# Performance work log

Hardware: AMD Instinct MI355X
Metric: run time of the kernel (lower is better)

## Reference

```python
import jax, jax.numpy as jnp
import numpy as np

B, L, T, E, H = 64, 256, 32, 384, 6
DI, DS, DC, DR = 768, 16, 4, 24  # d_inner, d_state, d_conv, dt_rank
HID, V, ND = 1536, 97, 12       # ffn hidden, num_classes, mamba depth
EPS = 1e-5


def setup_inputs() -> dict:
    key = jax.random.key(0)
    ks = jax.random.split(key, 16)
    n = lambda i, shape, s=0.02: jax.random.normal(ks[i], shape, jnp.float32) * s
    # sinusoidal position table (deterministic buffer)
    pos = np.arange(T)[:, None]
    i = np.arange(E)[None, :]
    ang = pos / np.power(10000.0, 2 * (i // 2) / E)
    pos_emb = jnp.asarray(np.where(i % 2 == 0, np.sin(ang), np.cos(ang)), jnp.float32)
    # standard S4D-real init for A_log
    Alog = jnp.log(jnp.broadcast_to(jnp.arange(1, DS + 1, dtype=jnp.float32), (ND, DI, DS)))
    return {
        'enc': jax.random.normal(ks[0], (B, L, E), jnp.float32),
        'query_embed': n(1, (1, T, E)),
        'pos_emb': pos_emb,
        'm_norm_w': jnp.ones((ND, E)),
        'm_in_w': n(2, (ND, 2 * DI, E)),
        'm_conv_w': n(3, (ND, DI, DC), 0.3),
        'm_conv_b': jnp.zeros((ND, DI)),
        'm_xproj_w': n(4, (ND, DR + 2 * DS, DI)),
        'm_dt_w': n(5, (ND, DI, DR), 0.1),
        'm_dt_b': n(6, (ND, DI), 0.5),
        'm_Alog': Alog,
        'm_D': jnp.ones((ND, DI)),
        'm_out_w': n(7, (ND, E, DI)),
        'rms_w': jnp.ones((E,)),
        'wq': n(8, (E, E)), 'bq': jnp.zeros((E,)),
        'wk': n(9, (E, E)), 'bk': jnp.zeros((E,)),
        'wv': n(10, (E, E)), 'bv': jnp.zeros((E,)),
        'wo': n(11, (E, E)), 'bo': jnp.zeros((E,)),
        'ln1_w': jnp.ones((E,)), 'ln1_b': jnp.zeros((E,)),
        'ffn_w1': n(12, (HID, E)), 'ffn_b1': jnp.zeros((HID,)),
        'ffn_w2': n(13, (E, HID)), 'ffn_b2': jnp.zeros((E,)),
        'ln2_w': jnp.ones((E,)), 'ln2_b': jnp.zeros((E,)),
        'out_w': n(14, (V, E)), 'out_b': jnp.zeros((V,)),
    }


def _rmsnorm(x, w):
    x = x.astype(jnp.float32)
    return x * jax.lax.rsqrt(jnp.mean(x * x, -1, keepdims=True) + EPS) * w


def _layernorm(x, w, b):
    x = x.astype(jnp.float32)
    mu = jnp.mean(x, -1, keepdims=True)
    var = jnp.mean((x - mu) ** 2, -1, keepdims=True)
    return (x - mu) * jax.lax.rsqrt(var + EPS) * w + b


def _mamba(x, in_w, conv_w, conv_b, xproj_w, dt_w, dt_b, Alog, Dp, ow):
    # x: (B, T, E)
    xz = jnp.einsum('bte,de->btd', x, in_w)
    xm, z = jnp.split(xz, 2, axis=-1)              # (B, T, DI) each
    t = xm.shape[1]
    xpad = jnp.pad(xm, ((0, 0), (DC - 1, 0), (0, 0)))  # causal depthwise conv
    xc = sum(conv_w[:, k] * xpad[:, k:k + t, :] for k in range(DC)) + conv_b
    xc = jax.nn.silu(xc)
    dbl = jnp.einsum('btd,rd->btr', xc, xproj_w)
    dt = jax.nn.softplus(jnp.einsum('btr,dr->btd', dbl[..., :DR], dt_w) + dt_b)
    Bm = dbl[..., DR:DR + DS]                      # (B, T, DS)
    Cm = dbl[..., DR + DS:]                        # (B, T, DS)
    A = -jnp.exp(Alog)                             # (DI, DS)
    dA = jnp.exp(dt[..., None] * A)                # (B, T, DI, DS)
    dBx = dt[..., None] * Bm[:, :, None, :] * xc[..., None]

    def step(h, inp):
        dA_t, dBx_t, C_t = inp
        h = dA_t * h + dBx_t                       # (B, DI, DS)
        return h, jnp.einsum('bds,bs->bd', h, C_t)

    h0 = jnp.zeros((xm.shape[0], DI, DS), jnp.float32)
    _, ys = jax.lax.scan(step, h0, (dA.transpose(1, 0, 2, 3), dBx.transpose(1, 0, 2, 3), Cm.transpose(1, 0, 2)))
    y = ys.transpose(1, 0, 2) + Dp * xc
    y = y * jax.nn.silu(z)
    return jnp.einsum('btd,ed->bte', y, ow)


def _block(carry, p):
    hidden, residual = carry
    norm_w, in_w, conv_w, conv_b, xproj_w, dt_w, dt_b, Alog, Dp, ow = p
    residual = hidden.astype(jnp.float32) + residual   # fused add-norm, residual_in_fp32
    hidden = _rmsnorm(residual, norm_w)
    hidden = _mamba(hidden, in_w, conv_w, conv_b, xproj_w, dt_w, dt_b, Alog, Dp, ow)
    return (hidden, residual), None


def reference(enc, query_embed, pos_emb, m_norm_w, m_in_w, m_conv_w, m_conv_b,
              m_xproj_w, m_dt_w, m_dt_b, m_Alog, m_D, m_out_w, rms_w,
              wq, bq, wk, bk, wv, bv, wo, bo, ln1_w, ln1_b,
              ffn_w1, ffn_b1, ffn_w2, ffn_b2, ln2_w, ln2_b, out_w, out_b):
    b = enc.shape[0]
    q = jnp.broadcast_to(query_embed, (b,) + query_embed.shape[1:]) + pos_emb  # (B, T, E)

    carry = (q, jnp.zeros_like(q))
    (hidden, residual), _ = jax.lax.scan(
        jax.checkpoint(_block), carry,
        (m_norm_w, m_in_w, m_conv_w, m_conv_b, m_xproj_w, m_dt_w, m_dt_b, m_Alog, m_D, m_out_w))

    # final fused RMSNorm (prenorm)
    residual = hidden + residual
    hidden = _rmsnorm(residual, rms_w)

    # cross attention: query=hidden, key=value=enc
    hd = E // H
    qh = (hidden @ wq.T + bq).reshape(b, T, H, hd)
    kh = (enc @ wk.T + bk).reshape(b, L, H, hd)
    vh = (enc @ wv.T + bv).reshape(b, L, H, hd)
    scores = jnp.einsum('bthd,bshd->bhts', qh, kh) / jnp.sqrt(jnp.float32(hd))
    attn = jax.nn.softmax(scores, axis=-1)
    ctx = jnp.einsum('bhts,bshd->bthd', attn, vh).reshape(b, T, E)
    ctx = ctx @ wo.T + bo

    residual = residual + ctx
    hidden = _layernorm(residual, ln1_w, ln1_b)

    ff = jax.nn.relu(hidden @ ffn_w1.T + ffn_b1) @ ffn_w2.T + ffn_b2
    residual = residual + ff
    hidden = _layernorm(residual, ln2_w, ln2_b)

    logits = hidden @ out_w.T + out_b              # (B, T, V)
    return logits
```

## Files before the change

### kernel.cpp

```cpp
#include <hip/hip_runtime.h>
#include <math.h>

constexpr int B_ = 64, L_ = 256, T_ = 32, E_ = 384, H_ = 6;
constexpr int DI_ = 768, DS_ = 16, DC_ = 4, DR_ = 24;
constexpr int HID_ = 1536, V_ = 97, ND_ = 12;
constexpr float EPS_ = 1e-5f;
constexpr int HD_ = 64;

typedef unsigned short ushort_t;
typedef __attribute__((ext_vector_type(8))) short  short8;
typedef __attribute__((ext_vector_type(4))) float  floatx4;
typedef __attribute__((ext_vector_type(8))) unsigned short ushort8v;

__device__ __forceinline__ float siluf(float x) { return x / (1.f + __expf(-x)); }
__device__ __forceinline__ float softplusf(float x) {
    return fmaxf(x, 0.f) + log1pf(expf(-fabsf(x)));
}
__device__ __forceinline__ ushort_t f2bf(float f) {
    unsigned int u = __float_as_uint(f);
    u += 0x7fffu + ((u >> 16) & 1u);
    return (ushort_t)(u >> 16);
}
__device__ __forceinline__ float bf2f(ushort_t u) {
    return __uint_as_float(((unsigned int)u) << 16);
}
__device__ __forceinline__ void unpack2(unsigned int w, float& lo, float& hi) {
    lo = __uint_as_float(w << 16);
    hi = __uint_as_float(w & 0xffff0000u);
}
__device__ __forceinline__ void gl_lds16(const ushort_t* g, ushort_t* l) {
    __builtin_amdgcn_global_load_lds(
        (const __attribute__((address_space(1))) unsigned int*)g,
        (__attribute__((address_space(3))) unsigned int*)l, 16, 0, 0);
}

__global__ __launch_bounds__(256) void cvt_bf16_kernel(
    const float* __restrict__ src, ushort_t* __restrict__ dst, long n4) {
    long i = (long)blockIdx.x * 256 + threadIdx.x;
    if (i >= n4) return;
    float4 v = ((const float4*)src)[i];
    __attribute__((ext_vector_type(4))) unsigned short o;
    o[0] = f2bf(v.x); o[1] = f2bf(v.y); o[2] = f2bf(v.z); o[3] = f2bf(v.w);
    *(__attribute__((ext_vector_type(4))) unsigned short*)(dst + i * 4) = o;
}

__global__ __launch_bounds__(256) void cvt_pad_kernel(
    const float* __restrict__ src, ushort_t* __restrict__ dst,
    int sr, int sc, int dr, int dc, int layers) {
    long total = (long)layers * dr * dc;
    long idx = (long)blockIdx.x * 256 + threadIdx.x;
    if (idx >= total) return;
    int l = (int)(idx / ((long)dr * dc));
    int rem = (int)(idx % ((long)dr * dc));
    int r = rem / dc, c = rem % dc;
    float v = (r < sr && c < sc) ? src[((long)l * sr + r) * sc + c] : 0.f;
    dst[idx] = f2bf(v);
}

template <int ACT, int OBF>
__global__ __launch_bounds__(256) void gemm_bf16(
    const ushort_t* __restrict__ A, int lda,
    const ushort_t* __restrict__ W,
    const float* __restrict__ bias,
    const float* __restrict__ addin,
    void* __restrict__ Cv,
    int M, int N, int K, int Nz, int ldc) {
    __shared__ ushort_t As[64 * 64];
    __shared__ ushort_t Bs[64 * 64];

    const int tid = threadIdx.x;
    const int wv = tid >> 6, ln = tid & 63;
    const int bm = blockIdx.x * 64, bn = blockIdx.y * 64;
    const int lm = ln & 15, quad = ln >> 4;
    const int wm = (wv & 1) * 32, wn = (wv >> 1) * 32;
    const int r8 = ln >> 3, c8 = ln & 7;

    floatx4 acc[2][2] = {};

    for (int k0 = 0; k0 < K; k0 += 64) {
#pragma unroll
        for (int j = 0; j < 2; ++j) {
            int row = wv * 16 + j * 8 + r8;
            int cg = c8 ^ (row & 7);
            gl_lds16(A + (size_t)(bm + row) * lda + k0 + cg * 8,
                     &As[(wv * 16 + j * 8) * 64]);
        }
#pragma unroll
        for (int j = 0; j < 2; ++j) {
            int row = wv * 16 + j * 8 + r8;
            int cg = c8 ^ (row & 7);
            gl_lds16(W + (size_t)(bn + row) * K + k0 + cg * 8,
                     &Bs[(wv * 16 + j * 8) * 64]);
        }
        __syncthreads();
#pragma unroll
        for (int ks2 = 0; ks2 < 2; ++ks2) {
            int pc = ((quad + ks2 * 4) ^ (lm & 7)) * 8;
            short8 a0 = *(const short8*)&As[(wm + lm) * 64 + pc];
            short8 a1 = *(const short8*)&As[(wm + 16 + lm) * 64 + pc];
            short8 b0 = *(const short8*)&Bs[(wn + lm) * 64 + pc];
            short8 b1 = *(const short8*)&Bs[(wn + 16 + lm) * 64 + pc];
            acc[0][0] = __builtin_amdgcn_mfma_f32_16x16x32_bf16(a0, b0, acc[0][0], 0, 0, 0);
            acc[0][1] = __builtin_amdgcn_mfma_f32_16x16x32_bf16(a0, b1, acc[0][1], 0, 0, 0);
            acc[1][0] = __builtin_amdgcn_mfma_f32_16x16x32_bf16(a1, b0, acc[1][0], 0, 0, 0);
            acc[1][1] = __builtin_amdgcn_mfma_f32_16x16x32_bf16(a1, b1, acc[1][1], 0, 0, 0);
        }
        __syncthreads();
    }

#pragma unroll
    for (int sm = 0; sm < 2; ++sm) {
#pragma unroll
        for (int sn = 0; sn < 2; ++sn) {
            const int gn = bn + wn + sn * 16 + lm;
            if (gn >= Nz) continue;
#pragma unroll
            for (int r = 0; r < 4; ++r) {
                const int gm = bm + wm + sm * 16 + quad * 4 + r;
                float v;
                if (gn < N) {
                    v = acc[sm][sn][r];
                    if (bias) v += bias[gn];
                    if (ACT == 1) v = fmaxf(v, 0.f);
                    if (ACT == 2) v = softplusf(v);
                    if (addin) v += addin[(size_t)gm * ldc + gn];
                } else {
                    v = 0.f;
                }
                if (OBF)
                    ((ushort_t*)Cv)[(size_t)gm * ldc + gn] = f2bf(v);
                else
                    ((float*)Cv)[(size_t)gm * ldc + gn] = v;
            }
        }
    }
}

__global__ __launch_bounds__(256) void gemm_in_conv(
    const ushort_t* __restrict__ A,
    const ushort_t* __restrict__ W,
    const float* __restrict__ cw,
    const float* __restrict__ cb,
    ushort_t* __restrict__ xz,
    ushort_t* __restrict__ xc) {
    __shared__ ushort_t As[64 * 64];
    __shared__ ushort_t Bs[64 * 64];
    __shared__ float Cb[64][65];
    __shared__ float Cw[64][4];
    __shared__ float Cbias[64];

    const int tid = threadIdx.x;
    const int wv = tid >> 6, ln = tid & 63;
    const int bm = blockIdx.x * 64, bn = blockIdx.y * 64;
    const int lm = ln & 15, quad = ln >> 4;
    const int wm = (wv & 1) * 32, wn = (wv >> 1) * 32;
    const int r8 = ln >> 3, c8 = ln & 7;
    const bool is_xm = (bn < DI_);

    if (is_xm && tid < 64) {
        *(float4*)&Cw[tid][0] = *(const float4*)&cw[(bn + tid) * 4];
        Cbias[tid] = cb[bn + tid];
    }

    floatx4 acc[2][2] = {};

    for (int k0 = 0; k0 < E_; k0 += 64) {
#pragma unroll
        for (int j = 0; j < 2; ++j) {
            int row = wv * 16 + j * 8 + r8;
            int cg = c8 ^ (row & 7);
            gl_lds16(A + (size_t)(bm + row) * E_ + k0 + cg * 8,
                     &As[(wv * 16 + j * 8) * 64]);
        }
#pragma unroll
        for (int j = 0; j < 2; ++j) {
            int row = wv * 16 + j * 8 + r8;
            int cg = c8 ^ (row & 7);
            gl_lds16(W + (size_t)(bn + row) * E_ + k0 + cg * 8,
                     &Bs[(wv * 16 + j * 8) * 64]);
        }
        __syncthreads();
#pragma unroll
        for (int ks2 = 0; ks2 < 2; ++ks2) {
            int pc = ((quad + ks2 * 4) ^ (lm & 7)) * 8;
            short8 a0 = *(const short8*)&As[(wm + lm) * 64 + pc];
            short8 a1 = *(const short8*)&As[(wm + 16 + lm) * 64 + pc];
            short8 b0 = *(const short8*)&Bs[(wn + lm) * 64 + pc];
            short8 b1 = *(const short8*)&Bs[(wn + 16 + lm) * 64 + pc];
            acc[0][0] = __builtin_amdgcn_mfma_f32_16x16x32_bf16(a0, b0, acc[0][0], 0, 0, 0);
            acc[0][1] = __builtin_amdgcn_mfma_f32_16x16x32_bf16(a0, b1, acc[0][1], 0, 0, 0);
            acc[1][0] = __builtin_amdgcn_mfma_f32_16x16x32_bf16(a1, b0, acc[1][0], 0, 0, 0);
            acc[1][1] = __builtin_amdgcn_mfma_f32_16x16x32_bf16(a1, b1, acc[1][1], 0, 0, 0);
        }
        __syncthreads();
    }

    if (is_xm) {
#pragma unroll
        for (int sm = 0; sm < 2; ++sm)
#pragma unroll
            for (int sn = 0; sn < 2; ++sn)
#pragma unroll
                for (int r = 0; r < 4; ++r)
                    Cb[wm + sm * 16 + quad * 4 + r][wn + sn * 16 + lm] = acc[sm][sn][r];
        __syncthreads();
        const int r = tid >> 2, c0 = (tid & 3) * 16;
        const int tl = r & 31;
        ushort_t pk[16];
#pragma unroll
        for (int j = 0; j < 16; ++j) {
            const int c = c0 + j;
            float a = Cbias[c];
#pragma unroll
            for (int k = 0; k < DC_; ++k) {
                int rr = tl + k - (DC_ - 1);
                if (rr >= 0) a += Cw[c][k] * Cb[r + k - (DC_ - 1)][c];
            }
            pk[j] = f2bf(siluf(a));
        }
        ushort_t* dst = xc + (size_t)(bm + r) * DI_ + bn + c0;
        *(ushort8v*)dst = *(ushort8v*)&pk[0];
        *(ushort8v*)(dst + 8) = *(ushort8v*)&pk[8];
    } else {
#pragma unroll
        for (int sm = 0; sm < 2; ++sm)
#pragma unroll
            for (int sn = 0; sn < 2; ++sn) {
                const int gn = bn + wn + sn * 16 + lm;
#pragma unroll
                for (int r = 0; r < 4; ++r) {
                    const int gm = bm + wm + sm * 16 + quad * 4 + r;
                    xz[(size_t)gm * 1536 + gn] = f2bf(acc[sm][sn][r]);
                }
            }
    }
}

__global__ __launch_bounds__(256) void xproj_dt_scan_kernel(
    const ushort_t* __restrict__ xc,
    const ushort_t* __restrict__ xz,
    const ushort_t* __restrict__ w_xproj,
    const float* __restrict__ dt_w,
    const float* __restrict__ dt_b,
    const float* __restrict__ Alog,
    const float* __restrict__ Dp,
    ushort_t* __restrict__ y) {
    __shared__ ushort_t Xs[32 * 768];
    __shared__ float Dbl[32][64];

    const int tid = threadIdx.x;
    const int wv = tid >> 6, ln = tid & 63;
    const int b = blockIdx.y;
    const int lm = ln & 15, quad = ln >> 4;
    const int r8 = ln >> 3, c8 = ln & 7;

#pragma unroll
    for (int i = 0; i < 12; ++i) {
        int q = wv * 96 + i * 8 + r8;
        int row = q / 12, chunk = q % 12;
        int cg = c8 ^ (row & 7);
        gl_lds16(xc + (size_t)(b * T_ + row) * DI_ + chunk * 64 + cg * 8,
                 &Xs[(wv * 96 + i * 8) * 64]);
    }
    __syncthreads();

    {
        const int mt = wv & 1, nt0 = wv >> 1;
        floatx4 a0 = {}, a1 = {};
        const int arow = mt * 16 + lm;
#pragma unroll
        for (int ks = 0; ks < 24; ++ks) {
            int og = (((ks & 1) * 4 + quad) ^ (arow & 7)) * 8;
            short8 av = *(const short8*)&Xs[(arow * 12 + (ks >> 1)) * 64 + og];
            short8 b0 = *(const short8*)(w_xproj + (size_t)(nt0 * 16 + lm) * DI_ +
                                         ks * 32 + quad * 8);
            short8 b1 = *(const short8*)(w_xproj + (size_t)((nt0 + 2) * 16 + lm) * DI_ +
                                         ks * 32 + quad * 8);
            a0 = __builtin_amdgcn_mfma_f32_16x16x32_bf16(av, b0, a0, 0, 0, 0);
            a1 = __builtin_amdgcn_mfma_f32_16x16x32_bf16(av, b1, a1, 0, 0, 0);
        }
#pragma unroll
        for (int r = 0; r < 4; ++r) {
            Dbl[mt * 16 + quad * 4 + r][nt0 * 16 + lm] = a0[r];
            Dbl[mt * 16 + quad * 4 + r][(nt0 + 2) * 16 + lm] = a1[r];
        }
    }
    __syncthreads();

    const int d = blockIdx.x * 256 + tid;
    float wdt[DR_];
#pragma unroll
    for (int r = 0; r < DR_; ++r) wdt[r] = dt_w[(size_t)d * DR_ + r];
    const float dtb_v = dt_b[d];
    float Aa[DS_];
#pragma unroll
    for (int s = 0; s < DS_; ++s) Aa[s] = -expf(Alog[(size_t)d * DS_ + s]);
    const float Dv = Dp[d];
    float h[DS_] = {};

    const int chunk64 = d >> 6, off = d & 63, elem = off & 7;
    for (int t = 0; t < T_; ++t) {
        float dtv = dtb_v;
#pragma unroll
        for (int r4 = 0; r4 < DR_ / 4; ++r4) {
            float4 dv = *(const float4*)&Dbl[t][r4 * 4];
            dtv += dv.x * wdt[r4 * 4] + dv.y * wdt[r4 * 4 + 1] +
                   dv.z * wdt[r4 * 4 + 2] + dv.w * wdt[r4 * 4 + 3];
        }
        dtv = softplusf(dtv);

        int og = ((off >> 3) ^ (t & 7)) * 8;
        float xcv = bf2f(Xs[(t * 12 + chunk64) * 64 + og + elem]);

        float acc = 0.f;
#pragma unroll
        for (int s4 = 0; s4 < DS_ / 4; ++s4) {
            float4 Bv = *(const float4*)&Dbl[t][DR_ + s4 * 4];
            float4 Cv = *(const float4*)&Dbl[t][DR_ + DS_ + s4 * 4];
#pragma unroll
            for (int j = 0; j < 4; ++j) {
                int s = s4 * 4 + j;
                float Bvj = (j == 0) ? Bv.x : (j == 1) ? Bv.y : (j == 2) ? Bv.z : Bv.w;
                float Cvj = (j == 0) ? Cv.x : (j == 1) ? Cv.y : (j == 2) ? Cv.z : Cv.w;
                h[s] = __expf(dtv * Aa[s]) * h[s] + dtv * Bvj * xcv;
                acc += h[s] * Cvj;
            }
        }
        float zv = bf2f(xz[(size_t)(b * T_ + t) * (2 * DI_) + DI_ + d]);
        y[(size_t)(b * T_ + t) * DI_ + d] = f2bf((acc + Dv * xcv) * siluf(zv));
    }
}

__global__ void init_kernel(const float* __restrict__ qe,
                            const float* __restrict__ pos,
                            float* __restrict__ houtf,
                            float* __restrict__ residual) {
    long idx = (long)blockIdx.x * 256 + threadIdx.x;
    if (idx >= (long)B_ * T_ * E_) return;
    int te = (int)(idx % ((long)T_ * E_));
    houtf[idx] = qe[te] + pos[te];
    residual[idx] = 0.f;
}

__global__ __launch_bounds__(256) void add_rmsnorm_kernel(
    const float* __restrict__ hin, float* __restrict__ residual,
    ushort_t* __restrict__ hout, const float* __restrict__ w) {
    const int row = blockIdx.x, tid = threadIdx.x;
    const long base = (long)row * E_;
    __shared__ float ws[4];

    float x0 = hin[base + tid] + residual[base + tid];
    bool has1 = (tid + 256 < E_);
    float x1 = has1 ? hin[base + tid + 256] + residual[base + tid + 256] : 0.f;
    residual[base + tid] = x0;
    if (has1) residual[base + tid + 256] = x1;

    float p = x0 * x0 + x1 * x1;
#pragma unroll
    for (int m = 1; m < 64; m <<= 1) p += __shfl_xor(p, m, 64);
    if ((tid & 63) == 0) ws[tid >> 6] = p;
    __syncthreads();
    float sc = rsqrtf((ws[0] + ws[1] + ws[2] + ws[3]) / E_ + EPS_);
    hout[base + tid] = f2bf(x0 * sc * w[tid]);
    if (has1) hout[base + tid + 256] = f2bf(x1 * sc * w[tid + 256]);
}

__global__ __launch_bounds__(256) void layernorm_kernel(
    const float* __restrict__ x, const float* __restrict__ w,
    const float* __restrict__ b, ushort_t* __restrict__ out) {
    const int row = blockIdx.x, tid = threadIdx.x;
    const long base = (long)row * E_;
    __shared__ float wa[4], wb[4];

    float x0 = x[base + tid];
    bool has1 = (tid + 256 < E_);
    float x1 = has1 ? x[base + tid + 256] : 0.f;

    float p = x0 + x1;
#pragma unroll
    for (int m = 1; m < 64; m <<= 1) p += __shfl_xor(p, m, 64);
    if ((tid & 63) == 0) wa[tid >> 6] = p;
    __syncthreads();
    float mu = (wa[0] + wa[1] + wa[2] + wa[3]) / E_;

    float d0 = x0 - mu, d1 = has1 ? x1 - mu : 0.f;
    float q = d0 * d0 + d1 * d1;
#pragma unroll
    for (int m = 1; m < 64; m <<= 1) q += __shfl_xor(q, m, 64);
    if ((tid & 63) == 0) wb[tid >> 6] = q;
    __syncthreads();
    float sc = rsqrtf((wb[0] + wb[1] + wb[2] + wb[3]) / E_ + EPS_);
    out[base + tid] = f2bf(d0 * sc * w[tid] + b[tid]);
    if (has1) out[base + tid + 256] = f2bf(d1 * sc * w[tid + 256] + b[tid + 256]);
}

__global__ __launch_bounds__(256) void attn_kernel(
    const ushort_t* __restrict__ qh,
    const ushort_t* __restrict__ kh,
    const ushort_t* __restrict__ vh,
    ushort_t* __restrict__ ctx) {
    const int h = blockIdx.x % H_;
    const int b = blockIdx.x / H_;
    const int tid = threadIdx.x;
    const int w = tid >> 6, ln = tid & 63;
    const int lm = ln & 15, quad = ln >> 4;

    __shared__ __attribute__((aligned(16))) ushort_t Vt[64 * 264];
    __shared__ __attribute__((aligned(16))) ushort_t Pb[32 * 264];
    __shared__ float rmax[4][32];
    __shared__ float rsum[4][32];

    short8 aq[2][2];
#pragma unroll
    for (int mt = 0; mt < 2; ++mt)
#pragma unroll
        for (int ks = 0; ks < 2; ++ks)
            aq[mt][ks] = *(const short8*)(qh + (size_t)(b * T_ + mt * 16 + lm) * E_ +
                                          h * HD_ + ks * 32 + quad * 8);

    short8 bk[4][2];
#pragma unroll
    for (int nt = 0; nt < 4; ++nt)
#pragma unroll
        for (int ks = 0; ks < 2; ++ks)
            bk[nt][ks] = *(const short8*)(kh + (size_t)(b * L_ + w * 64 + nt * 16 + lm) * E_ +
                                          h * HD_ + ks * 32 + quad * 8);

    {
        const int sp = tid & 127, dh = tid >> 7;
        const int s0 = sp * 2;
        const ushort_t* vr = vh + (size_t)(b * L_ + s0) * E_ + h * HD_ + dh * 32;
        uint4 va[4], vb[4];
#pragma unroll
        for (int c = 0; c < 4; ++c) {
            va[c] = *(const uint4*)(vr + c * 8);
            vb[c] = *(const uint4*)(vr + E_ + c * 8);
        }
#pragma unroll
        for (int c = 0; c < 4; ++c) {
            const unsigned int* pa = (const unsigned int*)&va[c];
            const unsigned int* pb = (const unsigned int*)&vb[c];
#pragma unroll
            for (int j = 0; j < 4; ++j) {
                int d0 = dh * 32 + c * 8 + j * 2;
                unsigned int lo = (pa[j] & 0xffffu) | (pb[j] << 16);
                unsigned int hi = (pa[j] >> 16) | (pb[j] & 0xffff0000u);
                *(unsigned int*)&Vt[d0 * 264 + s0] = lo;
                *(unsigned int*)&Vt[(d0 + 1) * 264 + s0] = hi;
            }
        }
    }

    floatx4 acc[2][4] = {};
#pragma unroll
    for (int ks = 0; ks < 2; ++ks)
#pragma unroll
        for (int mt = 0; mt < 2; ++mt)
#pragma unroll
            for (int nt = 0; nt < 4; ++nt)
                acc[mt][nt] = __builtin_amdgcn_mfma_f32_16x16x32_bf16(
                    aq[mt][ks], bk[nt][ks], acc[mt][nt], 0, 0, 0);
#pragma unroll
    for (int mt = 0; mt < 2; ++mt)
#pragma unroll
        for (int nt = 0; nt < 4; ++nt)
            acc[mt][nt] *= 0.125f;

    float mpart[2][4];
#pragma unroll
    for (int mt = 0; mt < 2; ++mt)
#pragma unroll
        for (int r = 0; r < 4; ++r) {
            float m = fmaxf(fmaxf(acc[mt][0][r], acc[mt][1][r]),
                            fmaxf(acc[mt][2][r], acc[mt][3][r]));
#pragma unroll
            for (int mk = 1; mk < 16; mk <<= 1)
                m = fmaxf(m, __shfl_xor(m, mk, 64));
            mpart[mt][r] = m;
        }
    if (lm == 0) {
#pragma unroll
        for (int mt = 0; mt < 2; ++mt)
#pragma unroll
            for (int r = 0; r < 4; ++r)
                rmax[w][mt * 16 + quad * 4 + r] = mpart[mt][r];
    }
    __syncthreads();

    float spart[2][4];
#pragma unroll
    for (int mt = 0; mt < 2; ++mt)
#pragma unroll
        for (int r = 0; r < 4; ++r) {
            const int t = mt * 16 + quad * 4 + r;
            float gm = fmaxf(fmaxf(rmax[0][t], rmax[1][t]),
                             fmaxf(rmax[2][t], rmax[3][t]));
            float s = 0.f;
#pragma unroll
            for (int nt = 0; nt < 4; ++nt) {
                float e = __expf(acc[mt][nt][r] - gm);
                s += e;
                Pb[t * 264 + w * 64 + nt * 16 + lm] = f2bf(e);
            }
#pragma unroll
            for (int mk = 1; mk < 16; mk <<= 1)
                s += __shfl_xor(s, mk, 64);
            spart[mt][r] = s;
        }
    if (lm == 0) {
#pragma unroll
        for (int mt = 0; mt < 2; ++mt)
#pragma unroll
            for (int r = 0; r < 4; ++r)
                rsum[w][mt * 16 + quad * 4 + r] = spart[mt][r];
    }
    __syncthreads();

    const int mt = w & 1, nth = w >> 1;
    floatx4 pacc[2] = {};
#pragma unroll
    for (int ks = 0; ks < 8; ++ks) {
        short8 pa = *(const short8*)&Pb[(mt * 16 + lm) * 264 + ks * 32 + quad * 8];
#pragma unroll
        for (int i = 0; i < 2; ++i) {
            short8 vb = *(const short8*)&Vt[((nth * 2 + i) * 16 + lm) * 264 + ks * 32 + quad * 8];
            pacc[i] = __builtin_amdgcn_mfma_f32_16x16x32_bf16(pa, vb, pacc[i], 0, 0, 0);
        }
    }

#pragma unroll
    for (int r = 0; r < 4; ++r) {
        const int t = mt * 16 + quad * 4 + r;
        float dn = 1.f / (rsum[0][t] + rsum[1][t] + rsum[2][t] + rsum[3][t]);
#pragma unroll
        for (int i = 0; i < 2; ++i) {
            const int d = (nth * 2 + i) * 16 + lm;
            ctx[(size_t)(b * T_ + t) * E_ + h * HD_ + d] = f2bf(pacc[i][r] * dn);
        }
    }
}

static void gemm(hipStream_t s, int act, int obf, const ushort_t* A, int lda,
                 const ushort_t* W, const float* bias, const float* addin,
                 void* C, int M, int N, int K, int Nz, int ldc) {
    dim3 g(M / 64, (Nz + 63) / 64), b(256);
    if (obf) {
        switch (act) {
            case 0: gemm_bf16<0, 1><<<g, b, 0, s>>>(A, lda, W, bias, addin, C, M, N, K, Nz, ldc); break;
            case 1: gemm_bf16<1, 1><<<g, b, 0, s>>>(A, lda, W, bias, addin, C, M, N, K, Nz, ldc); break;
            case 2: gemm_bf16<2, 1><<<g, b, 0, s>>>(A, lda, W, bias, addin, C, M, N, K, Nz, ldc); break;
        }
    } else {
        gemm_bf16<0, 0><<<g, b, 0, s>>>(A, lda, W, bias, addin, C, M, N, K, Nz, ldc);
    }
}

static void cvt(hipStream_t s, const float* src, ushort_t* dst, long n) {
    long n4 = n / 4;
    cvt_bf16_kernel<<<(int)((n4 + 255) / 256), 256, 0, s>>>(src, dst, n4);
}
static void cvt_pad(hipStream_t s, const float* src, ushort_t* dst,
                    int sr, int sc, int dr, int dc, int layers) {
    long total = (long)layers * dr * dc;
    cvt_pad_kernel<<<(int)((total + 255) / 256), 256, 0, s>>>(src, dst, sr, sc, dr, dc, layers);
}

extern "C" void kernel_launch(void* const* d_in, const int* in_sizes, int n_in,
                              void* d_out, int out_size, void* d_ws, size_t ws_size,
                              hipStream_t stream) {
    const float* enc      = (const float*)d_in[0];
    const float* qe       = (const float*)d_in[1];
    const float* pos      = (const float*)d_in[2];
    const float* m_norm_w = (const float*)d_in[3];
    const float* m_in_w   = (const float*)d_in[4];
    const float* m_conv_w = (const float*)d_in[5];
    const float* m_conv_b = (const float*)d_in[6];
    const float* m_xproj_w= (const float*)d_in[7];
    const float* m_dt_w   = (const float*)d_in[8];
    const float* m_dt_b   = (const float*)d_in[9];
    const float* m_Alog   = (const float*)d_in[10];
    const float* m_D      = (const float*)d_in[11];
    const float* m_out_w  = (const float*)d_in[12];
    const float* rms_w    = (const float*)d_in[13];
    const float* wq = (const float*)d_in[14];
    const float* bq = (const float*)d_in[15];
    const float* wk = (const float*)d_in[16];
    const float* bk = (const float*)d_in[17];
    const float* wv = (const float*)d_in[18];
    const float* bv = (const float*)d_in[19];
    const float* wo = (const float*)d_in[20];
    const float* bo = (const float*)d_in[21];
    const float* ln1_w = (const float*)d_in[22];
    const float* ln1_b = (const float*)d_in[23];
    const float* ffn_w1 = (const float*)d_in[24];
    const float* ffn_b1 = (const float*)d_in[25];
    const float* ffn_w2 = (const float*)d_in[26];
    const float* ffn_b2 = (const float*)d_in[27];
    const float* ln2_w = (const float*)d_in[28];
    const float* ln2_b = (const float*)d_in[29];
    const float* out_w = (const float*)d_in[30];
    const float* out_b = (const float*)d_in[31];

    const long SZ_BTE = (long)B_ * T_ * E_;
    float* residual = (float*)d_ws;
    float* houtf    = residual + SZ_BTE;

    ushort_t* u = (ushort_t*)(houtf + SZ_BTE);
    ushort_t* hidden = u;
    ushort_t* S      = hidden + SZ_BTE;
    ushort_t* xz  = S;
    ushort_t* xc  = xz + 3145728;
    ushort_t* yb  = xc + 1572864;
    ushort_t* enc_bf = S;
    ushort_t* qh  = S + 6291456;
    ushort_t* ctx = qh + 786432;
    ushort_t* ffnb = S;
    ushort_t* kh = S + 7995392;
    ushort_t* vh = kh + 6291456;

    ushort_t* w_in    = vh + 6291456;
    ushort_t* w_xproj = w_in + 7077888;
    ushort_t* w_out   = w_xproj + 589824;
    ushort_t* w_q     = w_out + 3538944;
    ushort_t* w_k     = w_q + 147456;
    ushort_t* w_v     = w_k + 147456;
    ushort_t* w_o     = w_v + 147456;
    ushort_t* w_f1    = w_o + 147456;
    ushort_t* w_f2    = w_f1 + 589824;
    ushort_t* w_lg    = w_f2 + 589824;

    const int M  = B_ * T_;
    const int MK = B_ * L_;

    cvt(stream, m_in_w,  w_in,  7077888);
    cvt_pad(stream, m_xproj_w, w_xproj, 56, 768, 64, 768, 12);
    cvt(stream, m_out_w, w_out, 3538944);
    cvt(stream, wq, w_q, 147456);
    cvt(stream, wk, w_k, 147456);
    cvt(stream, wv, w_v, 147456);
    cvt(stream, wo, w_o, 147456);
    cvt(stream, ffn_w1, w_f1, 589824);
    cvt(stream, ffn_w2, w_f2, 589824);
    cvt_pad(stream, out_w, w_lg, 97, 384, 128, 384, 1);

    init_kernel<<<(int)((SZ_BTE + 255) / 256), 256, 0, stream>>>(qe, pos, houtf, residual);

    for (int l = 0; l < ND_; ++l) {
        add_rmsnorm_kernel<<<M, 256, 0, stream>>>(houtf, residual, hidden,
                                                  m_norm_w + (long)l * E_);
        gemm_in_conv<<<dim3(M / 64, 24), 256, 0, stream>>>(
            hidden, w_in + (long)l * 1536 * 384,
            m_conv_w + (long)l * DI_ * DC_, m_conv_b + (long)l * DI_, xz, xc);
        xproj_dt_scan_kernel<<<dim3(3, B_), 256, 0, stream>>>(
            xc, xz, w_xproj + (long)l * 64 * 768,
            m_dt_w + (long)l * DI_ * DR_, m_dt_b + (long)l * DI_,
            m_Alog + (long)l * DI_ * DS_, m_D + (long)l * DI_, yb);
        gemm(stream, 0, 0, yb, DI_, w_out + (long)l * 384 * 768,
             nullptr, nullptr, houtf, M, 384, 768, 384, 384);
    }

    add_rmsnorm_kernel<<<M, 256, 0, stream>>>(houtf, residual, hidden, rms_w);

    gemm(stream, 0, 1, hidden, E_, w_q, bq, nullptr, qh, M, 384, 384, 384, 384);
    cvt(stream, enc, enc_bf, (long)MK * E_);
    gemm(stream, 0, 1, enc_bf, E_, w_k, bk, nullptr, kh, MK, 384, 384, 384, 384);
    gemm(stream, 0, 1, enc_bf, E_, w_v, bv, nullptr, vh, MK, 384, 384, 384, 384);
    attn_kernel<<<B_ * H_, 256, 0, stream>>>(qh, kh, vh, ctx);
    gemm(stream, 0, 0, ctx, E_, w_o, bo, residual, residual, M, 384, 384, 384, 384);

    layernorm_kernel<<<M, 256, 0, stream>>>(residual, ln1_w, ln1_b, hidden);
    gemm(stream, 1, 1, hidden, E_, w_f1, ffn_b1, nullptr, ffnb, M, 1536, 384, 1536, 1536);
    gemm(stream, 0, 0, ffnb, HID_, w_f2, ffn_b2, residual, residual, M, 384, 1536, 384, 384);
    layernorm_kernel<<<M, 256, 0, stream>>>(residual, ln2_w, ln2_b, hidden);

    gemm(stream, 0, 0, hidden, E_, w_lg, out_b, nullptr, (float*)d_out, M, V_, 384, V_, V_);
}
```

Before: 984.6 us.

## Split scan state across four lanes per channel with shuffle reductions

The selective-scan kernel now gives each d_inner channel four threads, each holding four of the sixteen state elements and a quarter of the dt_rank dot product, with partial sums combined by xor shuffles. Blocks grow to 512 threads and the grid doubles to six channel blocks per batch. The x_proj MFMA work is spread over eight waves, so each wave computes one output tile. This is meant to raise parallelism and cut per-thread register use and serial work in the latency-bound scan. In exchange, every block reloads the Xs tile and recomputes the projection, twice as often as before, and the shuffles add overhead.

Result: slower. 1.362 ms (+38.3%).

```diff
diff --git a/kernel.cpp b/kernel.cpp
--- a/kernel.cpp
+++ b/kernel.cpp
@@ -236,7 +236,7 @@
     }
 }
 
-__global__ __launch_bounds__(256) void xproj_dt_scan_kernel(
+__global__ __launch_bounds__(512) void xproj_dt_scan_kernel(
     const ushort_t* __restrict__ xc,
     const ushort_t* __restrict__ xz,
     const ushort_t* __restrict__ w_xproj,
@@ -255,79 +255,72 @@
     const int r8 = ln >> 3, c8 = ln & 7;
 
 #pragma unroll
-    for (int i = 0; i < 12; ++i) {
-        int q = wv * 96 + i * 8 + r8;
+    for (int i = 0; i < 6; ++i) {
+        int q = wv * 48 + i * 8 + r8;
         int row = q / 12, chunk = q % 12;
         int cg = c8 ^ (row & 7);
         gl_lds16(xc + (size_t)(b * T_ + row) * DI_ + chunk * 64 + cg * 8,
-                 &Xs[(wv * 96 + i * 8) * 64]);
+                 &Xs[(wv * 48 + i * 8) * 64]);
     }
     __syncthreads();
 
     {
-        const int mt = wv & 1, nt0 = wv >> 1;
-        floatx4 a0 = {}, a1 = {};
+        const int mt = wv & 1, nt = wv >> 1;
+        floatx4 a0 = {};
         const int arow = mt * 16 + lm;
 #pragma unroll
         for (int ks = 0; ks < 24; ++ks) {
             int og = (((ks & 1) * 4 + quad) ^ (arow & 7)) * 8;
             short8 av = *(const short8*)&Xs[(arow * 12 + (ks >> 1)) * 64 + og];
-            short8 b0 = *(const short8*)(w_xproj + (size_t)(nt0 * 16 + lm) * DI_ +
+            short8 bv = *(const short8*)(w_xproj + (size_t)(nt * 16 + lm) * DI_ +
                                          ks * 32 + quad * 8);
-            short8 b1 = *(const short8*)(w_xproj + (size_t)((nt0 + 2) * 16 + lm) * DI_ +
-                                         ks * 32 + quad * 8);
-            a0 = __builtin_amdgcn_mfma_f32_16x16x32_bf16(av, b0, a0, 0, 0, 0);
-            a1 = __builtin_amdgcn_mfma_f32_16x16x32_bf16(av, b1, a1, 0, 0, 0);
-        }
-#pragma unroll
-        for (int r = 0; r < 4; ++r) {
-            Dbl[mt * 16 + quad * 4 + r][nt0 * 16 + lm] = a0[r];
-            Dbl[mt * 16 + quad * 4 + r][(nt0 + 2) * 16 + lm] = a1[r];
-        }
+            a0 = __builtin_amdgcn_mfma_f32_16x16x32_bf16(av, bv, a0, 0, 0, 0);
+        }
+#pragma unroll
+        for (int r = 0; r < 4; ++r)
+            Dbl[mt * 16 + quad * 4 + r][nt * 16 + lm] = a0[r];
     }
     __syncthreads();
 
-    const int d = blockIdx.x * 256 + tid;
-    float wdt[DR_];
-#pragma unroll
-    for (int r = 0; r < DR_; ++r) wdt[r] = dt_w[(size_t)d * DR_ + r];
+    const int dl = tid >> 2, g = tid & 3;
+    const int d = blockIdx.x * 128 + dl;
+
+    float wdt[6];
+#pragma unroll
+    for (int j = 0; j < 6; ++j) wdt[j] = dt_w[(size_t)d * DR_ + g + 4 * j];
     const float dtb_v = dt_b[d];
-    float Aa[DS_];
-#pragma unroll
-    for (int s = 0; s < DS_; ++s) Aa[s] = -expf(Alog[(size_t)d * DS_ + s]);
+    float Aa[4];
+#pragma unroll
+    for (int j = 0; j < 4; ++j) Aa[j] = -expf(Alog[(size_t)d * DS_ + g * 4 + j]);
     const float Dv = Dp[d];
-    float h[DS_] = {};
+    float h[4] = {};
 
     const int chunk64 = d >> 6, off = d & 63, elem = off & 7;
     for (int t = 0; t < T_; ++t) {
-        float dtv = dtb_v;
-#pragma unroll
-        for (int r4 = 0; r4 < DR_ / 4; ++r4) {
-            float4 dv = *(const float4*)&Dbl[t][r4 * 4];
-            dtv += dv.x * wdt[r4 * 4] + dv.y * wdt[r4 * 4 + 1] +
-                   dv.z * wdt[r4 * 4 + 2] + dv.w * wdt[r4 * 4 + 3];
-        }
-        dtv = softplusf(dtv);
+        float dot = 0.f;
+#pragma unroll
+        for (int j = 0; j < 6; ++j) dot += Dbl[t][g + 4 * j] * wdt[j];
+        dot += __shfl_xor(dot, 1, 64);
+        dot += __shfl_xor(dot, 2, 64);
+        float dtv = softplusf(dot + dtb_v);
 
         int og = ((off >> 3) ^ (t & 7)) * 8;
         float xcv = bf2f(Xs[(t * 12 + chunk64) * 64 + og + elem]);
 
-        float acc = 0.f;
-#pragma unroll
-        for (int s4 = 0; s4 < DS_ / 4; ++s4) {
-            float4 Bv = *(const float4*)&Dbl[t][DR_ + s4 * 4];
-            float4 Cv = *(const float4*)&Dbl[t][DR_ + DS_ + s4 * 4];
-#pragma unroll
-            for (int j = 0; j < 4; ++j) {
-                int s = s4 * 4 + j;
-                float Bvj = (j == 0) ? Bv.x : (j == 1) ? Bv.y : (j == 2) ? Bv.z : Bv.w;
-                float Cvj = (j == 0) ? Cv.x : (j == 1) ? Cv.y : (j == 2) ? Cv.z : Cv.w;
-                h[s] = __expf(dtv * Aa[s]) * h[s] + dtv * Bvj * xcv;
-                acc += h[s] * Cvj;
-            }
-        }
-        float zv = bf2f(xz[(size_t)(b * T_ + t) * (2 * DI_) + DI_ + d]);
-        y[(size_t)(b * T_ + t) * DI_ + d] = f2bf((acc + Dv * xcv) * siluf(zv));
+        float4 Bv = *(const float4*)&Dbl[t][DR_ + g * 4];
+        float4 Cv = *(const float4*)&Dbl[t][DR_ + DS_ + g * 4];
+        float acc;
+        h[0] = __expf(dtv * Aa[0]) * h[0] + dtv * Bv.x * xcv; acc  = h[0] * Cv.x;
+        h[1] = __expf(dtv * Aa[1]) * h[1] + dtv * Bv.y * xcv; acc += h[1] * Cv.y;
+        h[2] = __expf(dtv * Aa[2]) * h[2] + dtv * Bv.z * xcv; acc += h[2] * Cv.z;
+        h[3] = __expf(dtv * Aa[3]) * h[3] + dtv * Bv.w * xcv; acc += h[3] * Cv.w;
+        acc += __shfl_xor(acc, 1, 64);
+        acc += __shfl_xor(acc, 2, 64);
+
+        if (g == 0) {
+            float zv = bf2f(xz[(size_t)(b * T_ + t) * (2 * DI_) + DI_ + d]);
+            y[(size_t)(b * T_ + t) * DI_ + d] = f2bf((acc + Dv * xcv) * siluf(zv));
+        }
     }
 }
 
@@ -651,7 +644,7 @@
         gemm_in_conv<<<dim3(M / 64, 24), 256, 0, stream>>>(
             hidden, w_in + (long)l * 1536 * 384,
             m_conv_w + (long)l * DI_ * DC_, m_conv_b + (long)l * DI_, xz, xc);
-        xproj_dt_scan_kernel<<<dim3(3, B_), 256, 0, stream>>>(
+        xproj_dt_scan_kernel<<<dim3(6, B_), 512, 0, stream>>>(
             xc, xz, w_xproj + (long)l * 64 * 768,
             m_dt_w + (long)l * DI_ * DR_, m_dt_b + (long)l * DI_,
             m_Alog + (long)l * DI_ * DS_, m_D + (long)l * DI_, yb);
```
